# Optimization experiments

Measured on AMD Instinct MI355X. Metric: run time of the kernel, lower is better.

The kernel has to match this reference:

```python
import jax, jax.numpy as jnp
import numpy as np

N_NODES = 100000
NEG_SLOPE = 0.2


def _gat_conv(x, edge_index, W, att_src, att_dst, bias):
    """Single-head PyG-style GATConv with self-loops.
    x: [N, F_in], edge_index: [2, E] (row 0 = src j, row 1 = dst i).
    """
    N = x.shape[0]
    h = x @ W  # [N, F_out]
    # add self-loops
    loop = jnp.arange(N, dtype=edge_index.dtype)
    src = jnp.concatenate([edge_index[0], loop])
    dst = jnp.concatenate([edge_index[1], loop])
    # per-node attention terms, gathered per edge
    a_s = h @ att_src  # [N]
    a_d = h @ att_dst  # [N]
    e = jax.nn.leaky_relu(a_s[src] + a_d[dst], NEG_SLOPE)  # [E+N]
    # segment softmax over incoming edges of each destination
    m = jax.ops.segment_max(e, dst, num_segments=N)  # [N]
    m = jnp.where(jnp.isfinite(m), m, 0.0)
    p = jnp.exp(e - m[dst])
    denom = jax.ops.segment_sum(p, dst, num_segments=N)  # [N], >0 due to self-loops
    alpha = p / denom[dst]  # [E+N]
    # scatter-aggregate weighted source features
    out = jax.ops.segment_sum(h[src] * alpha[:, None], dst, num_segments=N)
    return out + bias


def setup_inputs() -> dict:
    key = jax.random.key(0)
    ks = jax.random.split(key, 12)
    F_in, H, C = 128, 64, 40
    x = jax.random.normal(ks[0], (N_NODES, F_in), dtype=jnp.float32)
    edge_index = jax.random.randint(ks[1], (2, 1600000), 0, N_NODES, dtype=jnp.int64)
    s1 = 1.0 / np.sqrt(F_in)
    s2 = 1.0 / np.sqrt(H)
    return {
        "x": x,
        "edge_index": edge_index,
        "W1": jax.random.uniform(ks[2], (F_in, H), jnp.float32, -s1, s1),
        "att_src1": jax.random.uniform(ks[3], (H,), jnp.float32, -s2, s2),
        "att_dst1": jax.random.uniform(ks[4], (H,), jnp.float32, -s2, s2),
        "b1": jnp.zeros((H,), jnp.float32),
        "W2": jax.random.uniform(ks[5], (H, C), jnp.float32, -s2, s2),
        "att_src2": jax.random.uniform(ks[6], (C,), jnp.float32, -1.0 / np.sqrt(C), 1.0 / np.sqrt(C)),
        "att_dst2": jax.random.uniform(ks[7], (C,), jnp.float32, -1.0 / np.sqrt(C), 1.0 / np.sqrt(C)),
        "b2": jnp.zeros((C,), jnp.float32),
    }


def reference(x, edge_index, W1, att_src1, att_dst1, b1, W2, att_src2, att_dst2, b2):
    h = _gat_conv(x, edge_index, W1, att_src1, att_dst1, b1)
    h = jax.nn.relu(h)
    # dropout is identity in eval mode
    out = _gat_conv(h, edge_index, W2, att_src2, att_dst2, b2)
    return out
```

## Files before the change

kernel.cpp:

```cpp
#include <hip/hip_runtime.h>
#include <math.h>


#define NEG_SLOPE 0.2f
#define BIN_SHIFT 10
#define BIN_NODES 1024
#define MAXBINS   128
#define CAPB      17408
#define K1_CHUNK  4096
#define MAXDEG    128
#define AGG_STRIDE 132
#define XS1 136

typedef _Float16 h4_t __attribute__((ext_vector_type(4)));
typedef _Float16 h8_t __attribute__((ext_vector_type(8)));
typedef float    f16x_t __attribute__((ext_vector_type(16)));

__device__ __forceinline__ float lrelu(float v) {
    return v > 0.f ? v : NEG_SLOPE * v;
}

__global__ __launch_bounds__(256) void prep_kernel(
    const float* __restrict__ W1, const float* __restrict__ W2,
    const float* __restrict__ as1, const float* __restrict__ ad1,
    const float* __restrict__ as2, const float* __restrict__ ad2,
    _Float16* __restrict__ w1t, _Float16* __restrict__ w2t,
    float* __restrict__ u1, float* __restrict__ v1)
{
    const int tid = threadIdx.x;
    if (blockIdx.x == 0) {
        for (int i = tid; i < 8192; i += 256) {
            int n = i >> 7, k = i & 127;
            w1t[i] = (_Float16)W1[k * 64 + n];
        }
        if (tid < 128) {
            float su = 0.f, sv = 0.f;
            for (int n = 0; n < 64; ++n) {
                float w = W1[tid * 64 + n];
                su += w * as1[n];
                sv += w * ad1[n];
            }
            u1[tid] = su; v1[tid] = sv;
        }
    } else {
        __shared__ float u2l[64], v2l[64];
        if (tid < 64) {
            float su = 0.f, sv = 0.f;
            for (int n = 0; n < 40; ++n) {
                float w = W2[tid * 40 + n];
                su += w * as2[n];
                sv += w * ad2[n];
            }
            u2l[tid] = su; v2l[tid] = sv;
        }
        __syncthreads();
        for (int i = tid; i < 4096; i += 256) {
            int n = i >> 6, k = i & 63;
            _Float16 o = (_Float16)0.f;
            if (n < 40)       o = (_Float16)W2[k * 40 + n];
            else if (n == 40) o = (_Float16)u2l[k];
            else if (n == 41) o = (_Float16)v2l[k];
            w2t[i] = o;
        }
    }
}

__global__ __launch_bounds__(256) void gemm1_bin_kernel(
    const float* __restrict__ x, const _Float16* __restrict__ w1t,
    const float* __restrict__ u1, const float* __restrict__ v1,
    _Float16* __restrict__ h, float* __restrict__ as_, float* __restrict__ ad_,
    int N, int gb,
    const int* __restrict__ src, const int* __restrict__ dst, int E, int nbins,
    int* __restrict__ bin_cursor, int* __restrict__ binned)
{
    __shared__ __align__(16) char smem[35840];
    const int tid = threadIdx.x;

    if (blockIdx.x < gb) {
        _Float16* Xs = (_Float16*)smem;
        _Float16* Wt = (_Float16*)(smem + 17408);
        float*    Us = (float*)(smem + 34816);
        float*    Vs = (float*)(smem + 35328);
        const int lane = tid & 63;
        const int w = tid >> 6;
        const int rh = w >> 1, ch = w & 1;
        const long rowbase = (long)blockIdx.x * 64;

        {
            const int4* s4 = (const int4*)w1t;
#pragma unroll
            for (int i = 0; i < 4; ++i) {
                int f = tid + i * 256;
                int n = f >> 4, c = f & 15;
                *(int4*)&Wt[n * XS1 + c * 8] = s4[f];
            }
        }
        {
            const float4* X4 = (const float4*)x;
            const long gmax = (long)N * 32;
#pragma unroll
            for (int i = 0; i < 8; ++i) {
                int f = tid + i * 256;
                int row = f >> 5, c4 = f & 31;
                long gi = (rowbase + row) * 32 + c4;
                float4 v = (gi < gmax) ? X4[gi] : make_float4(0.f, 0.f, 0.f, 0.f);
                h4_t hv;
                hv.x = (_Float16)v.x; hv.y = (_Float16)v.y;
                hv.z = (_Float16)v.z; hv.w = (_Float16)v.w;
                *(h4_t*)&Xs[row * XS1 + c4 * 4] = hv;
            }
        }
        if (tid < 128) Us[tid] = u1[tid];
        else { int t = tid - 128; Vs[t] = v1[t]; }
        __syncthreads();

        {
            const int arow = tid >> 2, apart = tid & 3;
            const _Float16* xr = &Xs[arow * XS1 + apart * 32];
            float ps = 0.f, pd = 0.f;
#pragma unroll
            for (int k = 0; k < 32; k += 4) {
                h4_t xv = *(const h4_t*)(xr + k);
                float4 uu = *(const float4*)&Us[apart * 32 + k];
                float4 vv = *(const float4*)&Vs[apart * 32 + k];
                float x0 = (float)xv.x, x1 = (float)xv.y, x2 = (float)xv.z, x3 = (float)xv.w;
                ps += x0 * uu.x + x1 * uu.y + x2 * uu.z + x3 * uu.w;
                pd += x0 * vv.x + x1 * vv.y + x2 * vv.z + x3 * vv.w;
            }
            ps += __shfl_xor(ps, 1); ps += __shfl_xor(ps, 2);
            pd += __shfl_xor(pd, 1); pd += __shfl_xor(pd, 2);
            if (apart == 0 && rowbase + arow < N) {
                as_[rowbase + arow] = ps;
                ad_[rowbase + arow] = pd;
            }
        }

        const int m = lane & 31, khalf = lane >> 5;
        const _Float16* ax = &Xs[(rh * 32 + m) * XS1 + khalf * 8];
        const _Float16* bx = &Wt[(ch * 32 + m) * XS1 + khalf * 8];

        f16x_t acc = {};
#pragma unroll
        for (int kc = 0; kc < 8; ++kc) {
            h8_t a = *(const h8_t*)(ax + kc * 16);
            h8_t b = *(const h8_t*)(bx + kc * 16);
            acc = __builtin_amdgcn_mfma_f32_32x32x16_f16(a, b, acc, 0, 0, 0);
        }

        const int col = ch * 32 + m;
#pragma unroll
        for (int r = 0; r < 16; ++r) {
            int rowl = (r & 3) + 8 * (r >> 2) + 4 * khalf;
            long grow = rowbase + rh * 32 + rowl;
            if (grow < N) h[grow * 64 + col] = (_Float16)acc[r];
        }
    } else {
        int* hist = (int*)smem;
        int* base = (int*)(smem + 512);
        int* lcur = (int*)(smem + 1024);
        const int e0 = (blockIdx.x - gb) * K1_CHUNK;

        int sreg[16], dreg[16];
#pragma unroll
        for (int k = 0; k < 16; ++k) {
            int e = e0 + tid + k * 256;
            bool ok = e < E;
            dreg[k] = ok ? dst[e] : -1;
            sreg[k] = ok ? src[e] : 0;
        }

        if (tid < nbins) hist[tid] = 0;
        __syncthreads();
#pragma unroll
        for (int k = 0; k < 16; ++k)
            if (dreg[k] >= 0) atomicAdd(&hist[dreg[k] >> BIN_SHIFT], 1);
        __syncthreads();
        if (tid < nbins) {
            int c = hist[tid];
            base[tid] = (c > 0) ? atomicAdd(&bin_cursor[tid], c) : 0;
            lcur[tid] = 0;
        }
        __syncthreads();
#pragma unroll
        for (int k = 0; k < 16; ++k) {
            if (dreg[k] >= 0) {
                int b = dreg[k] >> BIN_SHIFT;
                int o = atomicAdd(&lcur[b], 1);
                int pos = base[b] + o;
                if (pos < CAPB)
                    binned[b * CAPB + pos] =
                        (sreg[k] << BIN_SHIFT) | (dreg[k] & (BIN_NODES - 1));
            }
        }
    }
}

__global__ __launch_bounds__(128) void scan_kernel(
    const int* __restrict__ bin_cursor, int* __restrict__ bin_base, int nbins)
{
    __shared__ int a[MAXBINS];
    const int tid = threadIdx.x;
    int v = (tid < nbins) ? min(bin_cursor[tid], CAPB) : 0;
    a[tid] = v;
    __syncthreads();
#pragma unroll
    for (int ofs = 1; ofs < 128; ofs <<= 1) {
        int t = (tid >= ofs) ? a[tid - ofs] : 0;
        __syncthreads();
        a[tid] += t;
        __syncthreads();
    }
    if (tid < nbins) bin_base[tid] = a[tid] - v;
}

__global__ __launch_bounds__(1024) void fine_kernel(
    const int* __restrict__ bin_cursor, const int* __restrict__ bin_base,
    const int* __restrict__ binned,
    int* __restrict__ csr, int* __restrict__ rowptr, int N, int nbins)
{
    __shared__ int a[BIN_NODES];
    __shared__ int cur[BIN_NODES];
    const int b = blockIdx.x;
    const int tid = threadIdx.x;

    const int cnt = min(bin_cursor[b], CAPB);
    const int binbase = bin_base[b];
    const int nn = min(BIN_NODES, N - b * BIN_NODES);
    const int* __restrict__ brec = binned + (long)b * CAPB;

    a[tid] = 0;
    __syncthreads();

    for (int k = tid; k < cnt; k += 1024) {
        atomicAdd(&a[brec[k] & (BIN_NODES - 1)], 1);
    }
    __syncthreads();

    int v = a[tid];
#pragma unroll
    for (int ofs = 1; ofs < BIN_NODES; ofs <<= 1) {
        int t = (tid >= ofs) ? a[tid - ofs] : 0;
        __syncthreads();
        a[tid] += t;
        __syncthreads();
    }
    const int excl = a[tid] - v;

    if (tid < nn) rowptr[b * BIN_NODES + tid] = binbase + excl;
    cur[tid] = binbase + excl;
    if (b == nbins - 1 && tid == 0) rowptr[N] = binbase + cnt;
    __syncthreads();

    for (int k = tid; k < cnt; k += 1024) {
        int rec = brec[k];
        int pos = atomicAdd(&cur[rec & (BIN_NODES - 1)], 1);
        csr[pos] = rec >> BIN_SHIFT;
    }
}

#define XS2 72
__global__ __launch_bounds__(256) void gemm2_kernel(
    const _Float16* __restrict__ hin, const _Float16* __restrict__ w2t,
    _Float16* __restrict__ h2, float* __restrict__ as_, float* __restrict__ ad_,
    int N)
{
    __shared__ __align__(16) _Float16 Xs[64 * XS2];
    __shared__ __align__(16) _Float16 Wt[64 * XS2];
    const int tid = threadIdx.x;
    const int lane = tid & 63;
    const int w = tid >> 6;
    const int rh = w >> 1, ch = w & 1;
    const long rowbase = (long)blockIdx.x * 64;

    {
        const int4* s4 = (const int4*)w2t;
#pragma unroll
        for (int i = 0; i < 2; ++i) {
            int f = tid + i * 256;
            int n = f >> 3, c = f & 7;
            *(int4*)&Wt[n * XS2 + c * 8] = s4[f];
        }
    }
    {
        const h8_t* X8 = (const h8_t*)hin;
        const long gmax = (long)N * 8;
#pragma unroll
        for (int i = 0; i < 2; ++i) {
            int f = tid + i * 256;
            int row = f >> 3, c = f & 7;
            long gi = (rowbase + row) * 8 + c;
            h8_t v = {};
            if (gi < gmax) v = X8[gi];
#pragma unroll
            for (int j = 0; j < 8; ++j) v[j] = (v[j] > (_Float16)0.f) ? v[j] : (_Float16)0.f;
            *(h8_t*)&Xs[row * XS2 + c * 8] = v;
        }
    }
    __syncthreads();

    const int m = lane & 31, khalf = lane >> 5;
    const _Float16* ax = &Xs[(rh * 32 + m) * XS2 + khalf * 8];
    const _Float16* bx = &Wt[(ch * 32 + m) * XS2 + khalf * 8];

    f16x_t acc = {};
#pragma unroll
    for (int kc = 0; kc < 4; ++kc) {
        h8_t a = *(const h8_t*)(ax + kc * 16);
        h8_t b = *(const h8_t*)(bx + kc * 16);
        acc = __builtin_amdgcn_mfma_f32_32x32x16_f16(a, b, acc, 0, 0, 0);
    }

    const int col = ch * 32 + m;
#pragma unroll
    for (int r = 0; r < 16; ++r) {
        int rowl = (r & 3) + 8 * (r >> 2) + 4 * khalf;
        long grow = rowbase + rh * 32 + rowl;
        float v = acc[r];
        if (grow < N) {
            if (col < 40)       h2[grow * 40 + col] = (_Float16)v;
            else if (col == 40) as_[grow] = v;
            else if (col == 41) ad_[grow] = v;
        }
    }
}

template<int F, typename OT>
__global__ __launch_bounds__(256) void aggregate_kernel(
    const _Float16* __restrict__ h, const float* __restrict__ as_,
    const float* __restrict__ ad_, const int* __restrict__ rowptr,
    const int* __restrict__ csr, const float* __restrict__ bias,
    OT* __restrict__ out, int N)
{
    __shared__ int   Ss[16 * AGG_STRIDE];
    __shared__ float Ps[16 * AGG_STRIDE];
    const int tid = threadIdx.x;
    const int dl  = tid >> 4;
    const int sub = tid & 15;
    const int i = blockIdx.x * 16 + dl;
    const bool alive = (i < N);

    int r0 = 0, deg = 0;
    if (alive) {
        r0 = rowptr[i];
        deg = rowptr[i + 1] - r0;
        if (deg > MAXDEG) deg = MAXDEG;
    }
    const float adi    = alive ? ad_[i] : 0.f;
    const float e_self = alive ? lrelu(as_[i] + adi) : 0.f;

    int*   __restrict__ sp = &Ss[dl * AGG_STRIDE];
    float* __restrict__ pp = &Ps[dl * AGG_STRIDE];

    float psum = 0.f;
    for (int c = sub; c < deg; c += 16) {
        int s = csr[r0 + c];
        float p = __expf(lrelu(as_[s] + adi));
        sp[c] = s;
        pp[c] = p;
        psum += p;
    }
#pragma unroll
    for (int off = 1; off < 16; off <<= 1) psum += __shfl_xor(psum, off);
    const float p_self = __expf(e_self);
    const float inv = 1.f / (psum + p_self);

    const bool act = (sub * 4 < F);
    const int  col = act ? sub * 4 : 0;
    float4 acc = make_float4(0.f, 0.f, 0.f, 0.f);

    int k = 0;
    for (; k + 4 <= deg; k += 4) {
        int   sA = sp[k],     sB = sp[k + 1], sC = sp[k + 2], sD = sp[k + 3];
        float pA = pp[k],     pB = pp[k + 1], pC = pp[k + 2], pD = pp[k + 3];
        if (act) {
            h4_t hA = *(const h4_t*)&h[(long)sA * F + col];
            h4_t hB = *(const h4_t*)&h[(long)sB * F + col];
            h4_t hC = *(const h4_t*)&h[(long)sC * F + col];
            h4_t hD = *(const h4_t*)&h[(long)sD * F + col];
            acc.x += (float)hA.x * pA + (float)hB.x * pB + (float)hC.x * pC + (float)hD.x * pD;
            acc.y += (float)hA.y * pA + (float)hB.y * pB + (float)hC.y * pC + (float)hD.y * pD;
            acc.z += (float)hA.z * pA + (float)hB.z * pB + (float)hC.z * pC + (float)hD.z * pD;
            acc.w += (float)hA.w * pA + (float)hB.w * pB + (float)hC.w * pC + (float)hD.w * pD;
        }
    }
    for (; k < deg; ++k) {
        int   s = sp[k];
        float p = pp[k];
        if (act) {
            h4_t hv = *(const h4_t*)&h[(long)s * F + col];
            acc.x += (float)hv.x * p; acc.y += (float)hv.y * p;
            acc.z += (float)hv.z * p; acc.w += (float)hv.w * p;
        }
    }

    if (alive && act) {
        h4_t hv = *(const h4_t*)&h[(long)i * F + col];
        float4 bv = *(const float4*)&bias[col];
        float ox = (acc.x + (float)hv.x * p_self) * inv + bv.x;
        float oy = (acc.y + (float)hv.y * p_self) * inv + bv.y;
        float oz = (acc.z + (float)hv.z * p_self) * inv + bv.z;
        float ow = (acc.w + (float)hv.w * p_self) * inv + bv.w;
        if constexpr (sizeof(OT) == 4) {
            float4 o = make_float4(ox, oy, oz, ow);
            *(float4*)&out[(long)i * F + col] = o;
        } else {
            h4_t o;
            o.x = (_Float16)ox; o.y = (_Float16)oy;
            o.z = (_Float16)oz; o.w = (_Float16)ow;
            *(h4_t*)&out[(long)i * F + col] = o;
        }
    }
}

extern "C" void kernel_launch(void* const* d_in, const int* in_sizes, int n_in,
                              void* d_out, int out_size, void* d_ws, size_t ws_size,
                              hipStream_t stream) {
    const float* x    = (const float*)d_in[0];
    const int*   ei   = (const int*)d_in[1];
    const float* W1   = (const float*)d_in[2];
    const float* at_s1= (const float*)d_in[3];
    const float* at_d1= (const float*)d_in[4];
    const float* b1   = (const float*)d_in[5];
    const float* W2   = (const float*)d_in[6];
    const float* at_s2= (const float*)d_in[7];
    const float* at_d2= (const float*)d_in[8];
    const float* b2   = (const float*)d_in[9];
    float* out = (float*)d_out;

    const int N = in_sizes[0] / 128;
    const int E = in_sizes[1] / 2;
    const int nbins = (N + BIN_NODES - 1) >> BIN_SHIFT;

    char* p = (char*)d_ws;
    auto carve = [&](size_t bytes) -> void* {
        void* r = (void*)p;
        p += (bytes + 255) & ~(size_t)255;
        return r;
    };
    int*       bin_cursor = (int*)      carve((size_t)MAXBINS * 4);
    int*       bin_base   = (int*)      carve((size_t)MAXBINS * 4);
    int*       binned     = (int*)      carve((size_t)nbins * CAPB * 4);
    int*       csr        = (int*)      carve((size_t)E * 4);
    int*       rowptr     = (int*)      carve((size_t)(N + 1) * 4);
    _Float16*  w1t        = (_Float16*) carve((size_t)8192 * 2);
    _Float16*  w2t        = (_Float16*) carve((size_t)4096 * 2);
    float*     u1         = (float*)    carve((size_t)128 * 4);
    float*     v1         = (float*)    carve((size_t)128 * 4);
    _Float16*  h1         = (_Float16*) carve((size_t)N * 64 * 2);
    _Float16*  agg1h      = (_Float16*) carve((size_t)N * 64 * 2);
    _Float16*  h2         = (_Float16*) carve((size_t)N * 40 * 2);
    float*     asn        = (float*)    carve((size_t)N * 4);
    float*     adn        = (float*)    carve((size_t)N * 4);

    hipMemsetAsync(bin_cursor, 0, (size_t)MAXBINS * 4, stream);

    prep_kernel<<<2, 256, 0, stream>>>(W1, W2, at_s1, at_d1, at_s2, at_d2,
                                       w1t, w2t, u1, v1);

    const int gb = (N + 63) / 64;
    const int bb = (E + K1_CHUNK - 1) / K1_CHUNK;
    gemm1_bin_kernel<<<gb + bb, 256, 0, stream>>>(
        x, w1t, u1, v1, h1, asn, adn, N, gb,
        ei, ei + E, E, nbins, bin_cursor, binned);

    scan_kernel<<<1, 128, 0, stream>>>(bin_cursor, bin_base, nbins);
    fine_kernel<<<nbins, 1024, 0, stream>>>(bin_cursor, bin_base, binned, csr, rowptr, N, nbins);

    aggregate_kernel<64, _Float16><<<(N + 15) / 16, 256, 0, stream>>>(
        h1, asn, adn, rowptr, csr, b1, agg1h, N);

    gemm2_kernel<<<(N + 63) / 64, 256, 0, stream>>>(agg1h, w2t, h2, asn, adn, N);

    aggregate_kernel<40, float><<<(N + 15) / 16, 256, 0, stream>>>(
        h2, asn, adn, rowptr, csr, b2, out, N);
}
```

Measured before the change: 241.4 us.

## Fuse layer-1 aggregation with GEMM2, drop scan kernel, keep weights in registers

```diff
diff --git a/kernel.cpp b/kernel.cpp
--- a/kernel.cpp
+++ b/kernel.cpp
@@ -11,6 +11,7 @@
 #define MAXDEG    128
 #define AGG_STRIDE 132
 #define XS1 136
+#define XS2 72
 
 typedef _Float16 h4_t __attribute__((ext_vector_type(4)));
 typedef _Float16 h8_t __attribute__((ext_vector_type(8)));
@@ -69,31 +70,29 @@
     const float* __restrict__ x, const _Float16* __restrict__ w1t,
     const float* __restrict__ u1, const float* __restrict__ v1,
     _Float16* __restrict__ h, float* __restrict__ as_, float* __restrict__ ad_,
-    int N, int gb,
+    int N, int bb,
     const int* __restrict__ src, const int* __restrict__ dst, int E, int nbins,
     int* __restrict__ bin_cursor, int* __restrict__ binned)
 {
-    __shared__ __align__(16) char smem[35840];
+    __shared__ __align__(16) char smem[18432];
     const int tid = threadIdx.x;
 
-    if (blockIdx.x < gb) {
+    if (blockIdx.x >= bb) {
         _Float16* Xs = (_Float16*)smem;
-        _Float16* Wt = (_Float16*)(smem + 17408);
-        float*    Us = (float*)(smem + 34816);
-        float*    Vs = (float*)(smem + 35328);
+        float*    Us = (float*)(smem + 17408);
+        float*    Vs = (float*)(smem + 17920);
         const int lane = tid & 63;
         const int w = tid >> 6;
         const int rh = w >> 1, ch = w & 1;
-        const long rowbase = (long)blockIdx.x * 64;
-
+        const int m = lane & 31, khalf = lane >> 5;
+        const long rowbase = (long)(blockIdx.x - bb) * 64;
+
+        h8_t bfrag[8];
         {
-            const int4* s4 = (const int4*)w1t;
-#pragma unroll
-            for (int i = 0; i < 4; ++i) {
-                int f = tid + i * 256;
-                int n = f >> 4, c = f & 15;
-                *(int4*)&Wt[n * XS1 + c * 8] = s4[f];
-            }
+            const _Float16* bp = w1t + (ch * 32 + m) * 128 + khalf * 8;
+#pragma unroll
+            for (int kc = 0; kc < 8; ++kc)
+                bfrag[kc] = *(const h8_t*)(bp + kc * 16);
         }
         {
             const float4* X4 = (const float4*)x;
@@ -135,16 +134,12 @@
             }
         }
 
-        const int m = lane & 31, khalf = lane >> 5;
         const _Float16* ax = &Xs[(rh * 32 + m) * XS1 + khalf * 8];
-        const _Float16* bx = &Wt[(ch * 32 + m) * XS1 + khalf * 8];
-
         f16x_t acc = {};
 #pragma unroll
         for (int kc = 0; kc < 8; ++kc) {
             h8_t a = *(const h8_t*)(ax + kc * 16);
-            h8_t b = *(const h8_t*)(bx + kc * 16);
-            acc = __builtin_amdgcn_mfma_f32_32x32x16_f16(a, b, acc, 0, 0, 0);
+            acc = __builtin_amdgcn_mfma_f32_32x32x16_f16(a, bfrag[kc], acc, 0, 0, 0);
         }
 
         const int col = ch * 32 + m;
@@ -158,7 +153,7 @@
         int* hist = (int*)smem;
         int* base = (int*)(smem + 512);
         int* lcur = (int*)(smem + 1024);
-        const int e0 = (blockIdx.x - gb) * K1_CHUNK;
+        const int e0 = blockIdx.x * K1_CHUNK;
 
         int sreg[16], dreg[16];
 #pragma unroll
@@ -195,27 +190,8 @@
     }
 }
 
-__global__ __launch_bounds__(128) void scan_kernel(
-    const int* __restrict__ bin_cursor, int* __restrict__ bin_base, int nbins)
-{
-    __shared__ int a[MAXBINS];
-    const int tid = threadIdx.x;
-    int v = (tid < nbins) ? min(bin_cursor[tid], CAPB) : 0;
-    a[tid] = v;
-    __syncthreads();
-#pragma unroll
-    for (int ofs = 1; ofs < 128; ofs <<= 1) {
-        int t = (tid >= ofs) ? a[tid - ofs] : 0;
-        __syncthreads();
-        a[tid] += t;
-        __syncthreads();
-    }
-    if (tid < nbins) bin_base[tid] = a[tid] - v;
-}
-
 __global__ __launch_bounds__(1024) void fine_kernel(
-    const int* __restrict__ bin_cursor, const int* __restrict__ bin_base,
-    const int* __restrict__ binned,
+    const int* __restrict__ bin_cursor, const int* __restrict__ binned,
     int* __restrict__ csr, int* __restrict__ rowptr, int N, int nbins)
 {
     __shared__ int a[BIN_NODES];
@@ -224,7 +200,9 @@
     const int tid = threadIdx.x;
 
     const int cnt = min(bin_cursor[b], CAPB);
-    const int binbase = bin_base[b];
+    int binbase = 0;
+    for (int j = 0; j < b; ++j) binbase += min(bin_cursor[j], CAPB);
+
     const int nn = min(BIN_NODES, N - b * BIN_NODES);
     const int* __restrict__ brec = binned + (long)b * CAPB;
 
@@ -258,78 +236,129 @@
     }
 }
 
-#define XS2 72
-__global__ __launch_bounds__(256) void gemm2_kernel(
-    const _Float16* __restrict__ hin, const _Float16* __restrict__ w2t,
-    _Float16* __restrict__ h2, float* __restrict__ as_, float* __restrict__ ad_,
+__global__ __launch_bounds__(256) void agg1_gemm2_kernel(
+    const _Float16* __restrict__ h1, const float* __restrict__ as_,
+    const float* __restrict__ ad_, const int* __restrict__ rowptr,
+    const int* __restrict__ csr, const float* __restrict__ b1,
+    const _Float16* __restrict__ w2t,
+    _Float16* __restrict__ h2, float* __restrict__ as2, float* __restrict__ ad2,
     int N)
 {
     __shared__ __align__(16) _Float16 Xs[64 * XS2];
-    __shared__ __align__(16) _Float16 Wt[64 * XS2];
+    __shared__ int   Ss[16 * AGG_STRIDE];
+    __shared__ float Ps[16 * AGG_STRIDE];
     const int tid = threadIdx.x;
+    const int dl  = tid >> 4;
+    const int sub = tid & 15;
     const int lane = tid & 63;
     const int w = tid >> 6;
     const int rh = w >> 1, ch = w & 1;
-    const long rowbase = (long)blockIdx.x * 64;
-
+    const int m = lane & 31, khalf = lane >> 5;
+
+    h8_t bfrag[4];
     {
-        const int4* s4 = (const int4*)w2t;
-#pragma unroll
-        for (int i = 0; i < 2; ++i) {
-            int f = tid + i * 256;
-            int n = f >> 3, c = f & 7;
-            *(int4*)&Wt[n * XS2 + c * 8] = s4[f];
-        }
-    }
-    {
-        const h8_t* X8 = (const h8_t*)hin;
-        const long gmax = (long)N * 8;
-#pragma unroll
-        for (int i = 0; i < 2; ++i) {
-            int f = tid + i * 256;
-            int row = f >> 3, c = f & 7;
-            long gi = (rowbase + row) * 8 + c;
-            h8_t v = {};
-            if (gi < gmax) v = X8[gi];
-#pragma unroll
-            for (int j = 0; j < 8; ++j) v[j] = (v[j] > (_Float16)0.f) ? v[j] : (_Float16)0.f;
-            *(h8_t*)&Xs[row * XS2 + c * 8] = v;
-        }
+        const _Float16* bp = w2t + (ch * 32 + m) * 64 + khalf * 8;
+#pragma unroll
+        for (int kc = 0; kc < 4; ++kc)
+            bfrag[kc] = *(const h8_t*)(bp + kc * 16);
+    }
+
+    int*   __restrict__ sp = &Ss[dl * AGG_STRIDE];
+    float* __restrict__ pp = &Ps[dl * AGG_STRIDE];
+    const float4 bv = *(const float4*)&b1[sub * 4];
+
+    for (int round = 0; round < 4; ++round) {
+        const int row = round * 16 + dl;
+        const int i = blockIdx.x * 64 + row;
+        const bool alive = (i < N);
+
+        int r0 = 0, deg = 0;
+        if (alive) {
+            r0 = rowptr[i];
+            deg = rowptr[i + 1] - r0;
+            if (deg > MAXDEG) deg = MAXDEG;
+        }
+        const float adi    = alive ? ad_[i] : 0.f;
+        const float e_self = alive ? lrelu(as_[i] + adi) : 0.f;
+
+        float psum = 0.f;
+        for (int c = sub; c < deg; c += 16) {
+            int s = csr[r0 + c];
+            float p = __expf(lrelu(as_[s] + adi));
+            sp[c] = s;
+            pp[c] = p;
+            psum += p;
+        }
+#pragma unroll
+        for (int off = 1; off < 16; off <<= 1) psum += __shfl_xor(psum, off);
+        const float p_self = __expf(e_self);
+        const float inv = 1.f / (psum + p_self);
+
+        const int col = sub * 4;
+        float4 acc = make_float4(0.f, 0.f, 0.f, 0.f);
+        int k = 0;
+        for (; k + 4 <= deg; k += 4) {
+            int   sA = sp[k],     sB = sp[k + 1], sC = sp[k + 2], sD = sp[k + 3];
+            float pA = pp[k],     pB = pp[k + 1], pC = pp[k + 2], pD = pp[k + 3];
+            h4_t hA = *(const h4_t*)&h1[(long)sA * 64 + col];
+            h4_t hB = *(const h4_t*)&h1[(long)sB * 64 + col];
+            h4_t hC = *(const h4_t*)&h1[(long)sC * 64 + col];
+            h4_t hD = *(const h4_t*)&h1[(long)sD * 64 + col];
+            acc.x += (float)hA.x * pA + (float)hB.x * pB + (float)hC.x * pC + (float)hD.x * pD;
+            acc.y += (float)hA.y * pA + (float)hB.y * pB + (float)hC.y * pC + (float)hD.y * pD;
+            acc.z += (float)hA.z * pA + (float)hB.z * pB + (float)hC.z * pC + (float)hD.z * pD;
+            acc.w += (float)hA.w * pA + (float)hB.w * pB + (float)hC.w * pC + (float)hD.w * pD;
+        }
+        for (; k < deg; ++k) {
+            int   s = sp[k];
+            float p = pp[k];
+            h4_t hv = *(const h4_t*)&h1[(long)s * 64 + col];
+            acc.x += (float)hv.x * p; acc.y += (float)hv.y * p;
+            acc.z += (float)hv.z * p; acc.w += (float)hv.w * p;
+        }
+
+        float ox = 0.f, oy = 0.f, oz = 0.f, ow = 0.f;
+        if (alive) {
+            h4_t hv = *(const h4_t*)&h1[(long)i * 64 + col];
+            ox = (acc.x + (float)hv.x * p_self) * inv + bv.x;
+            oy = (acc.y + (float)hv.y * p_self) * inv + bv.y;
+            oz = (acc.z + (float)hv.z * p_self) * inv + bv.z;
+            ow = (acc.w + (float)hv.w * p_self) * inv + bv.w;
+        }
+        h4_t o;
+        o.x = (_Float16)fmaxf(ox, 0.f); o.y = (_Float16)fmaxf(oy, 0.f);
+        o.z = (_Float16)fmaxf(oz, 0.f); o.w = (_Float16)fmaxf(ow, 0.f);
+        *(h4_t*)&Xs[row * XS2 + col] = o;
     }
     __syncthreads();
 
-    const int m = lane & 31, khalf = lane >> 5;
     const _Float16* ax = &Xs[(rh * 32 + m) * XS2 + khalf * 8];
-    const _Float16* bx = &Wt[(ch * 32 + m) * XS2 + khalf * 8];
-
-    f16x_t acc = {};
+    f16x_t acc2 = {};
 #pragma unroll
     for (int kc = 0; kc < 4; ++kc) {
         h8_t a = *(const h8_t*)(ax + kc * 16);
-        h8_t b = *(const h8_t*)(bx + kc * 16);
-        acc = __builtin_amdgcn_mfma_f32_32x32x16_f16(a, b, acc, 0, 0, 0);
+        acc2 = __builtin_amdgcn_mfma_f32_32x32x16_f16(a, bfrag[kc], acc2, 0, 0, 0);
     }
 
     const int col = ch * 32 + m;
 #pragma unroll
     for (int r = 0; r < 16; ++r) {
         int rowl = (r & 3) + 8 * (r >> 2) + 4 * khalf;
-        long grow = rowbase + rh * 32 + rowl;
-        float v = acc[r];
+        long grow = (long)blockIdx.x * 64 + rh * 32 + rowl;
+        float v = acc2[r];
         if (grow < N) {
             if (col < 40)       h2[grow * 40 + col] = (_Float16)v;
-            else if (col == 40) as_[grow] = v;
-            else if (col == 41) ad_[grow] = v;
-        }
-    }
-}
-
-template<int F, typename OT>
-__global__ __launch_bounds__(256) void aggregate_kernel(
+            else if (col == 40) as2[grow] = v;
+            else if (col == 41) ad2[grow] = v;
+        }
+    }
+}
+
+__global__ __launch_bounds__(256) void aggregate2_kernel(
     const _Float16* __restrict__ h, const float* __restrict__ as_,
     const float* __restrict__ ad_, const int* __restrict__ rowptr,
     const int* __restrict__ csr, const float* __restrict__ bias,
-    OT* __restrict__ out, int N)
+    float* __restrict__ out, int N)
 {
     __shared__ int   Ss[16 * AGG_STRIDE];
     __shared__ float Ps[16 * AGG_STRIDE];
@@ -364,7 +393,7 @@
     const float p_self = __expf(e_self);
     const float inv = 1.f / (psum + p_self);
 
-    const bool act = (sub * 4 < F);
+    const bool act = (sub * 4 < 40);
     const int  col = act ? sub * 4 : 0;
     float4 acc = make_float4(0.f, 0.f, 0.f, 0.f);
 
@@ -373,10 +402,10 @@
         int   sA = sp[k],     sB = sp[k + 1], sC = sp[k + 2], sD = sp[k + 3];
         float pA = pp[k],     pB = pp[k + 1], pC = pp[k + 2], pD = pp[k + 3];
         if (act) {
-            h4_t hA = *(const h4_t*)&h[(long)sA * F + col];
-            h4_t hB = *(const h4_t*)&h[(long)sB * F + col];
-            h4_t hC = *(const h4_t*)&h[(long)sC * F + col];
-            h4_t hD = *(const h4_t*)&h[(long)sD * F + col];
+            h4_t hA = *(const h4_t*)&h[(long)sA * 40 + col];
+            h4_t hB = *(const h4_t*)&h[(long)sB * 40 + col];
+            h4_t hC = *(const h4_t*)&h[(long)sC * 40 + col];
+            h4_t hD = *(const h4_t*)&h[(long)sD * 40 + col];
             acc.x += (float)hA.x * pA + (float)hB.x * pB + (float)hC.x * pC + (float)hD.x * pD;
             acc.y += (float)hA.y * pA + (float)hB.y * pB + (float)hC.y * pC + (float)hD.y * pD;
             acc.z += (float)hA.z * pA + (float)hB.z * pB + (float)hC.z * pC + (float)hD.z * pD;
@@ -387,28 +416,21 @@
         int   s = sp[k];
         float p = pp[k];
         if (act) {
-            h4_t hv = *(const h4_t*)&h[(long)s * F + col];
+            h4_t hv = *(const h4_t*)&h[(long)s * 40 + col];
             acc.x += (float)hv.x * p; acc.y += (float)hv.y * p;
             acc.z += (float)hv.z * p; acc.w += (float)hv.w * p;
         }
     }
 
     if (alive && act) {
-        h4_t hv = *(const h4_t*)&h[(long)i * F + col];
+        h4_t hv = *(const h4_t*)&h[(long)i * 40 + col];
         float4 bv = *(const float4*)&bias[col];
-        float ox = (acc.x + (float)hv.x * p_self) * inv + bv.x;
-        float oy = (acc.y + (float)hv.y * p_self) * inv + bv.y;
-        float oz = (acc.z + (float)hv.z * p_self) * inv + bv.z;
-        float ow = (acc.w + (float)hv.w * p_self) * inv + bv.w;
-        if constexpr (sizeof(OT) == 4) {
-            float4 o = make_float4(ox, oy, oz, ow);
-            *(float4*)&out[(long)i * F + col] = o;
-        } else {
-            h4_t o;
-            o.x = (_Float16)ox; o.y = (_Float16)oy;
-            o.z = (_Float16)oz; o.w = (_Float16)ow;
-            *(h4_t*)&out[(long)i * F + col] = o;
-        }
+        float4 o;
+        o.x = (acc.x + (float)hv.x * p_self) * inv + bv.x;
+        o.y = (acc.y + (float)hv.y * p_self) * inv + bv.y;
+        o.z = (acc.z + (float)hv.z * p_self) * inv + bv.z;
+        o.w = (acc.w + (float)hv.w * p_self) * inv + bv.w;
+        *(float4*)&out[(long)i * 40 + col] = o;
     }
 }
 
@@ -438,7 +460,6 @@
         return r;
     };
     int*       bin_cursor = (int*)      carve((size_t)MAXBINS * 4);
-    int*       bin_base   = (int*)      carve((size_t)MAXBINS * 4);
     int*       binned     = (int*)      carve((size_t)nbins * CAPB * 4);
     int*       csr        = (int*)      carve((size_t)E * 4);
     int*       rowptr     = (int*)      carve((size_t)(N + 1) * 4);
@@ -447,30 +468,28 @@
     float*     u1         = (float*)    carve((size_t)128 * 4);
     float*     v1         = (float*)    carve((size_t)128 * 4);
     _Float16*  h1         = (_Float16*) carve((size_t)N * 64 * 2);
-    _Float16*  agg1h      = (_Float16*) carve((size_t)N * 64 * 2);
     _Float16*  h2         = (_Float16*) carve((size_t)N * 40 * 2);
     float*     asn        = (float*)    carve((size_t)N * 4);
     float*     adn        = (float*)    carve((size_t)N * 4);
+    float*     asn2       = (float*)    carve((size_t)N * 4);
+    float*     adn2       = (float*)    carve((size_t)N * 4);
 
     hipMemsetAsync(bin_cursor, 0, (size_t)MAXBINS * 4, stream);
 
     prep_kernel<<<2, 256, 0, stream>>>(W1, W2, at_s1, at_d1, at_s2, at_d2,
                                        w1t, w2t, u1, v1);
 
+    const int bb = (E + K1_CHUNK - 1) / K1_CHUNK;
     const int gb = (N + 63) / 64;
-    const int bb = (E + K1_CHUNK - 1) / K1_CHUNK;
-    gemm1_bin_kernel<<<gb + bb, 256, 0, stream>>>(
-        x, w1t, u1, v1, h1, asn, adn, N, gb,
+    gemm1_bin_kernel<<<bb + gb, 256, 0, stream>>>(
+        x, w1t, u1, v1, h1, asn, adn, N, bb,
         ei, ei + E, E, nbins, bin_cursor, binned);
 
-    scan_kernel<<<1, 128, 0, stream>>>(bin_cursor, bin_base, nbins);
-    fine_kernel<<<nbins, 1024, 0, stream>>>(bin_cursor, bin_base, binned, csr, rowptr, N, nbins);
-
-    aggregate_kernel<64, _Float16><<<(N + 15) / 16, 256, 0, stream>>>(
-        h1, asn, adn, rowptr, csr, b1, agg1h, N);
-
-    gemm2_kernel<<<(N + 63) / 64, 256, 0, stream>>>(agg1h, w2t, h2, asn, adn, N);
-
-    aggregate_kernel<40, float><<<(N + 15) / 16, 256, 0, stream>>>(
-        h2, asn, adn, rowptr, csr, b2, out, N);
-}
+    fine_kernel<<<nbins, 1024, 0, stream>>>(bin_cursor, binned, csr, rowptr, N, nbins);
+
+    agg1_gemm2_kernel<<<(N + 63) / 64, 256, 0, stream>>>(
+        h1, asn, adn, rowptr, csr, b1, w2t, h2, asn2, adn2, N);
+
+    aggregate2_kernel<<<(N + 15) / 16, 256, 0, stream>>>(
+        h2, asn2, adn2, rowptr, csr, b2, out, N);
+}
```

Result: slower. 250.8 us (+3.9%).
